# Kernel optimization log

Hardware: AMD Instinct MI355X
Metric: run time of the kernel (lower is better)

## Reference

```python
import jax, jax.numpy as jnp
import numpy as np

N, D, H = 3072, 1152, 16
HD = D // H  # 72


def setup_inputs() -> dict:
    key = jax.random.key(0)
    ks = jax.random.split(key, 12)
    w = lambda k, shp: jax.random.normal(k, shp, dtype=jnp.float32) * 0.02
    return {
        "hidden_states": jax.random.normal(ks[0], (N, D), dtype=jnp.float32),
        "rotary_pos_emb": jax.random.normal(ks[1], (N, HD // 2), dtype=jnp.float32),
        "cu_seqlens": jnp.arange(5, dtype=jnp.int32) * (N // 4),
        "wq": w(ks[2], (D, D)), "bq": jnp.zeros((D,), jnp.float32),
        "wk": w(ks[3], (D, D)), "bk": jnp.zeros((D,), jnp.float32),
        "wv": w(ks[4], (D, D)), "bv": jnp.zeros((D,), jnp.float32),
        "wo": w(ks[5], (D, D)), "bo": jnp.zeros((D,), jnp.float32),
    }


def _rotate_half(x):
    x1, x2 = jnp.split(x, 2, axis=-1)
    return jnp.concatenate((-x2, x1), axis=-1)


def _apply_rope(t, freqs):
    # t: [N, H, HD], freqs: [N, HD//2]
    cos = jnp.concatenate([jnp.cos(freqs), jnp.cos(freqs)], axis=-1)[:, None, :]  # [N,1,HD]
    sin = jnp.concatenate([jnp.sin(freqs), jnp.sin(freqs)], axis=-1)[:, None, :]
    return (t.astype(jnp.float32) * cos + _rotate_half(t.astype(jnp.float32)) * sin).astype(t.dtype)


def reference(hidden_states, rotary_pos_emb, cu_seqlens, wq, bq, wk, bk, wv, bv, wo, bo):
    n = hidden_states.shape[0]
    q = (hidden_states @ wq.T + bq).reshape(n, H, HD)
    k = (hidden_states @ wk.T + bk).reshape(n, H, HD)
    v = (hidden_states @ wv.T + bv).reshape(n, H, HD)
    q = _apply_rope(q, rotary_pos_emb)
    k = _apply_rope(k, rotary_pos_emb)
    # block-diagonal mask: same segment id (from cu_seqlens) -> attend
    seg = jnp.searchsorted(cu_seqlens, jnp.arange(n), side="right")
    same = seg[:, None] == seg[None, :]  # [N, N]
    neg = jnp.finfo(q.dtype).min
    scores = jnp.einsum("qhd,khd->hqk", q, k) / jnp.sqrt(jnp.float32(HD)).astype(q.dtype)
    scores = scores + jnp.where(same, jnp.zeros((), q.dtype), neg)[None, :, :]
    attn = jax.nn.softmax(scores.astype(jnp.float32), axis=-1).astype(q.dtype)
    out = jnp.einsum("hqk,khd->qhd", attn, v).reshape(n, D)
    return out @ wo.T + bo
```

## Files before the change

### kernel.cpp

```cpp
#include <hip/hip_runtime.h>
#include <hip/hip_bf16.h>


typedef __attribute__((ext_vector_type(8))) __bf16 bf16x8;
typedef __attribute__((ext_vector_type(4))) float f32x4;
typedef __attribute__((ext_vector_type(8))) unsigned short u16x8;
typedef __attribute__((ext_vector_type(4))) unsigned short u16x4;
typedef __attribute__((ext_vector_type(4))) unsigned int u32x4;

#define N_TOK 3072
#define DMODEL 1152
#define NH 16
#define HDIM 72
#define SEGLEN 768

__device__ __forceinline__ unsigned short bf16rn(float f) {
  union { float f; unsigned int u; } v; v.f = f;
  return (unsigned short)((v.u + 0x7fffu + ((v.u >> 16) & 1u)) >> 16);
}
__device__ __forceinline__ float bf2f(unsigned short u) {
  union { unsigned int i; float f; } v; v.i = ((unsigned int)u) << 16;
  return v.f;
}

#define GLOAD16(gsrc, ldst)                                                  \
  __builtin_amdgcn_global_load_lds(                                         \
      (const __attribute__((address_space(1))) unsigned int*)(gsrc),        \
      (__attribute__((address_space(3))) unsigned int*)(ldst), 16, 0, 0)

template <int N> __device__ __forceinline__ void waitcnt_vm() {
  if constexpr (N == 0) asm volatile("s_waitcnt vmcnt(0)" ::: "memory");
  else if constexpr (N == 3) asm volatile("s_waitcnt vmcnt(3)" ::: "memory");
  else if constexpr (N == 4) asm volatile("s_waitcnt vmcnt(4)" ::: "memory");
}

__global__ __launch_bounds__(256) void prep_kernel(
    const float* __restrict__ hs, const float* __restrict__ rope,
    const float* __restrict__ wq, const float* __restrict__ wk,
    const float* __restrict__ wv, const float* __restrict__ wo,
    const float* __restrict__ bq, const float* __restrict__ bk,
    const float* __restrict__ bv,
    unsigned short* __restrict__ Xbf, unsigned short* __restrict__ Wqkv,
    unsigned short* __restrict__ Wo, float* __restrict__ biasqkv,
    float* __restrict__ csT, float* __restrict__ snT) {
  const int idx = blockIdx.x * 256 + threadIdx.x;
  const int stride = gridDim.x * 256;
  const int NX4 = (N_TOK * DMODEL) / 4;
  const int NW4 = (DMODEL * DMODEL) / 4;
  for (int i = idx; i < NX4; i += stride) {
    f32x4 v = ((const f32x4*)hs)[i];
    u16x4 o;
    for (int j = 0; j < 4; ++j) o[j] = bf16rn(v[j]);
    ((u16x4*)Xbf)[i] = o;
  }
  for (int i = idx; i < NW4; i += stride) {
    f32x4 a = ((const f32x4*)wq)[i];
    f32x4 b = ((const f32x4*)wk)[i];
    f32x4 c = ((const f32x4*)wv)[i];
    f32x4 d = ((const f32x4*)wo)[i];
    u16x4 oa, ob, oc, od;
    for (int j = 0; j < 4; ++j) {
      oa[j] = bf16rn(a[j]); ob[j] = bf16rn(b[j]);
      oc[j] = bf16rn(c[j]); od[j] = bf16rn(d[j]);
    }
    ((u16x4*)Wqkv)[i] = oa;
    ((u16x4*)(Wqkv + DMODEL * DMODEL))[i] = ob;
    ((u16x4*)(Wqkv + 2 * DMODEL * DMODEL))[i] = oc;
    ((u16x4*)Wo)[i] = od;
  }
  for (int i = idx; i < N_TOK * 36; i += stride) {
    const int n = i / 36, d = i - n * 36;
    const float f = rope[i];
    csT[n * 40 + d] = __cosf(f);
    snT[n * 40 + d] = __sinf(f);
  }
  for (int i = idx; i < DMODEL; i += stride) {
    biasqkv[i] = bq[i];
    biasqkv[DMODEL + i] = bk[i];
    biasqkv[2 * DMODEL + i] = bv[i];
  }
}

template <int BM, int BN, int FM, int FN, bool OBF>
__global__ __launch_bounds__(256) void gemm_lds_kernel(
    const unsigned short* __restrict__ A, const unsigned short* __restrict__ B,
    const float* __restrict__ bias, void* __restrict__ Cout,
    int Nout, int K, int nbx) {
  __shared__ unsigned short As[3][BM * 32];
  __shared__ unsigned short Bs[3][BN * 32];
  const int t = threadIdx.x;
  const int lane = t & 63, wave = t >> 6;
  const int wr = wave >> 1, wc = wave & 1;
  const int g = lane >> 4, li = lane & 15;
  constexpr int LPS = BM / 64 + BN / 64;

  const int per = gridDim.x >> 3;
  const int gb = (blockIdx.x & 7) * per + (blockIdx.x >> 3);
  const int by = gb / nbx, bx = gb - by * nbx;
  const int bm = by * BM, bn = bx * BN;

  constexpr int LA = BM / 64;
  constexpr int LB = BN / 64;

  auto stage = [&](int buf, int kt) {
#pragma unroll
    for (int i = 0; i < LA; ++i) {
      const int s = i * 256 + t;
      const int row = s >> 2, cs = s & 3;
      const int gg = cs ^ ((row >> 1) & 3);
      GLOAD16(A + (long)(bm + row) * K + kt + gg * 8,
              &As[buf][(i * 256 + (t & ~63)) * 8]);
    }
#pragma unroll
    for (int i = 0; i < LB; ++i) {
      const int s = i * 256 + t;
      const int row = s >> 2, cs = s & 3;
      const int gg = cs ^ ((row >> 1) & 3);
      GLOAD16(B + (long)(bn + row) * K + kt + gg * 8,
              &Bs[buf][(i * 256 + (t & ~63)) * 8]);
    }
  };

  f32x4 acc[FM][FN];
#pragma unroll
  for (int i = 0; i < FM; ++i)
#pragma unroll
    for (int j = 0; j < FN; ++j) acc[i][j] = (f32x4)0.f;

  stage(0, 0);
  stage(1, 32);
  int cur = 0;
  const int nk = K / 32;
  for (int kt = 0; kt < nk; ++kt) {
    if (kt < nk - 1) waitcnt_vm<LPS>();
    else waitcnt_vm<0>();
    __builtin_amdgcn_s_barrier();
    if (kt + 2 < nk) {
      int nb = cur + 2; if (nb >= 3) nb -= 3;
      stage(nb, (kt + 2) * 32);
    }
    bf16x8 af[FM], bf[FN];
#pragma unroll
    for (int i = 0; i < FM; ++i) {
      const int r = wr * (BM / 2) + i * 16 + li;
      af[i] = *(const bf16x8*)&As[cur][r * 32 + ((g ^ ((r >> 1) & 3)) * 8)];
    }
#pragma unroll
    for (int j = 0; j < FN; ++j) {
      const int r = wc * (BN / 2) + j * 16 + li;
      bf[j] = *(const bf16x8*)&Bs[cur][r * 32 + ((g ^ ((r >> 1) & 3)) * 8)];
    }
    __builtin_amdgcn_s_setprio(1);
#pragma unroll
    for (int i = 0; i < FM; ++i)
#pragma unroll
      for (int j = 0; j < FN; ++j)
        acc[i][j] = __builtin_amdgcn_mfma_f32_16x16x32_bf16(af[i], bf[j],
                                                            acc[i][j], 0, 0, 0);
    __builtin_amdgcn_s_setprio(0);
    cur = (cur == 2) ? 0 : cur + 1;
  }

#pragma unroll
  for (int i = 0; i < FM; ++i) {
    const int row = bm + wr * (BM / 2) + i * 16 + g * 4;
#pragma unroll
    for (int j = 0; j < FN; ++j) {
      const int col = bn + wc * (BN / 2) + j * 16 + li;
      const float bb = bias[col];
#pragma unroll
      for (int r = 0; r < 4; ++r) {
        const float v = acc[i][j][r] + bb;
        if constexpr (OBF)
          ((unsigned short*)Cout)[(long)(row + r) * Nout + col] = bf16rn(v);
        else
          ((float*)Cout)[(long)(row + r) * Nout + col] = v;
      }
    }
  }
}

__global__ __launch_bounds__(256) void rope_pack_kernel(
    const unsigned short* __restrict__ qkv, const float* __restrict__ csT,
    const float* __restrict__ snT, unsigned short* __restrict__ Qp,
    unsigned short* __restrict__ Kp, unsigned short* __restrict__ Vt) {
  const int nb = blockIdx.x;
  const int h = blockIdx.y;
  const int n0 = nb * 64;
  const int t = threadIdx.x;
  const float qscale = 0.17002501f;
  __shared__ float vtile[72][65];

  for (int i = t; i < 64 * 9; i += 256) {
    const int n = i / 9, dq = (i % 9) * 4;
    const long base = (long)(n0 + n) * 3456 + h * HDIM;
    f32x4 cv = *(const f32x4*)&csT[(long)(n0 + n) * 40 + dq];
    f32x4 sv = *(const f32x4*)&snT[(long)(n0 + n) * 40 + dq];
    u16x4 q1 = *(const u16x4*)&qkv[base + dq];
    u16x4 q2 = *(const u16x4*)&qkv[base + dq + 36];
    u16x4 k1 = *(const u16x4*)&qkv[base + DMODEL + dq];
    u16x4 k2 = *(const u16x4*)&qkv[base + DMODEL + dq + 36];
    u16x4 oq1, oq2, ok1, ok2;
#pragma unroll
    for (int e = 0; e < 4; ++e) {
      const float c = cv[e], s = sv[e];
      float f1 = bf2f(q1[e]), f2 = bf2f(q2[e]);
      oq1[e] = bf16rn((f1 * c - f2 * s) * qscale);
      oq2[e] = bf16rn((f2 * c + f1 * s) * qscale);
      f1 = bf2f(k1[e]); f2 = bf2f(k2[e]);
      ok1[e] = bf16rn(f1 * c - f2 * s);
      ok2[e] = bf16rn(f2 * c + f1 * s);
    }
    const long ob = ((long)h * N_TOK + n0 + n) * 96;
    *(u16x4*)&Qp[ob + dq] = oq1;
    *(u16x4*)&Qp[ob + dq + 36] = oq2;
    *(u16x4*)&Kp[ob + dq] = ok1;
    *(u16x4*)&Kp[ob + dq + 36] = ok2;
  }
  for (int i = t; i < 64 * 6; i += 256) {
    const int n = i / 6, dp = HDIM + (i % 6) * 4;
    const long ob = ((long)h * N_TOK + n0 + n) * 96;
    *(u16x4*)&Qp[ob + dp] = (u16x4)0;
    *(u16x4*)&Kp[ob + dp] = (u16x4)0;
  }
  for (int i = t; i < 64 * 9; i += 256) {
    const int n = i / 9, dq = (i % 9) * 8;
    u16x8 v = *(const u16x8*)&qkv[(long)(n0 + n) * 3456 + 2 * DMODEL + h * HDIM + dq];
#pragma unroll
    for (int e = 0; e < 8; ++e) vtile[dq + e][n] = bf2f(v[e]);
  }
  __syncthreads();
  for (int i = t; i < 80 * 8; i += 256) {
    const int d = i / 8, nq = (i % 8) * 8;
    u16x8 o;
#pragma unroll
    for (int e = 0; e < 8; ++e)
      o[e] = (d < HDIM) ? bf16rn(vtile[d][nq + e])
                        : (d == HDIM ? (unsigned short)0x3F80
                                     : (unsigned short)0);
    *(u16x8*)&Vt[((long)h * 80 + d) * N_TOK + n0 + nq] = o;
  }
}

__global__ __launch_bounds__(256) void attn_kernel(
    const unsigned short* __restrict__ Qp, const unsigned short* __restrict__ Kp,
    const unsigned short* __restrict__ Vt, unsigned short* __restrict__ AO) {
  const int b = blockIdx.x;
  const int hs = b & 63, qt = b >> 6;
  const int h = hs >> 2, seg = hs & 3;
  const int t = threadIdx.x;
  const int lane = t & 63, w = t >> 6;
  const int g = lane >> 4, li = lane & 15;

  __shared__ unsigned short Ks[2][32 * 96];
  __shared__ unsigned short Vs[2][80 * 32];

  const int q0 = seg * SEGLEN + qt * 64;
  const unsigned short* kbase = Kp + ((long)h * N_TOK + seg * SEGLEN) * 96;
  const unsigned short* vbase = Vt + (long)h * 80 * N_TOK + seg * SEGLEN;

  auto stageK = [&](int buf, int koff) {
    {
      const int row = t / 12, c = t - row * 12;
      const int gg = c ^ ((row >> 1) & 3);
      GLOAD16(kbase + (long)(koff + row) * 96 + gg * 8,
              &Ks[buf][(t & ~63) * 8]);
    }
    if (t < 128) {
      const int s = 256 + t;
      const int row = s / 12, c = s - row * 12;
      const int gg = c ^ ((row >> 1) & 3);
      GLOAD16(kbase + (long)(koff + row) * 96 + gg * 8,
              &Ks[buf][(256 + (t & ~63)) * 8]);
    }
  };
  auto stageV = [&](int buf, int koff) {
    {
      const int row = t >> 2, ch = t & 3;
      const int gg = ch ^ ((row >> 1) & 3);
      GLOAD16(vbase + (long)row * N_TOK + koff + gg * 8,
              &Vs[buf][(t & ~63) * 8]);
    }
    if (t < 64) {
      const int s = 256 + t;
      const int row = s >> 2, ch = s & 3;
      const int gg = ch ^ ((row >> 1) & 3);
      GLOAD16(vbase + (long)row * N_TOK + koff + gg * 8,
              &Vs[buf][(256 + (t & ~63)) * 8]);
    }
  };

  bf16x8 aq[3];
  {
    const unsigned short* qsrc = Qp + ((long)h * N_TOK + q0 + w * 16 + li) * 96;
#pragma unroll
    for (int c = 0; c < 3; ++c)
      aq[c] = *(const bf16x8*)(qsrc + c * 32 + g * 8);
  }

  const int a0 = (li + 32 * (g & 1)) << 2;
  const int a1 = a0 + 64;
  const bool glow = (g < 2);

  f32x4 accO[5];
#pragma unroll
  for (int j = 0; j < 5; ++j) accO[j] = (f32x4)0.f;

  stageK(0, 0);
  stageV(0, 0);
  int cur = 0;
  for (int kv = 0; kv < 24; ++kv) {
    __syncthreads();
    if (kv + 1 < 24) {
      stageK(cur ^ 1, (kv + 1) * 32);
      stageV(cur ^ 1, (kv + 1) * 32);
    }

    f32x4 sc[2];
#pragma unroll
    for (int f = 0; f < 2; ++f) sc[f] = (f32x4)0.f;
    __builtin_amdgcn_s_setprio(1);
#pragma unroll
    for (int c = 0; c < 3; ++c)
#pragma unroll
      for (int f = 0; f < 2; ++f) {
        const int kr = f * 16 + li;
        bf16x8 bk = *(const bf16x8*)
            &Ks[cur][kr * 96 + (((c * 4 + g) ^ ((kr >> 1) & 3)) * 8)];
        sc[f] = __builtin_amdgcn_mfma_f32_16x16x32_bf16(bk, aq[c], sc[f], 0, 0, 0);
      }
    __builtin_amdgcn_s_setprio(0);

    float p00 = exp2f(sc[0][0]), p01 = exp2f(sc[0][1]);
    float p02 = exp2f(sc[0][2]), p03 = exp2f(sc[0][3]);
    float p10 = exp2f(sc[1][0]), p11 = exp2f(sc[1][1]);
    float p12 = exp2f(sc[1][2]), p13 = exp2f(sc[1][3]);
    unsigned int pk00, pk01, pk10, pk11;
    asm("v_cvt_pk_bf16_f32 %0, %1, %2" : "=v"(pk00) : "v"(p00), "v"(p01));
    asm("v_cvt_pk_bf16_f32 %0, %1, %2" : "=v"(pk01) : "v"(p02), "v"(p03));
    asm("v_cvt_pk_bf16_f32 %0, %1, %2" : "=v"(pk10) : "v"(p10), "v"(p11));
    asm("v_cvt_pk_bf16_f32 %0, %1, %2" : "=v"(pk11) : "v"(p12), "v"(p13));

    u32x4 apv;
    {
      int t0 = __builtin_amdgcn_ds_bpermute(a0, (int)pk00);
      int t1 = __builtin_amdgcn_ds_bpermute(a0, (int)pk10);
      apv[0] = (unsigned int)(glow ? t0 : t1);
      t0 = __builtin_amdgcn_ds_bpermute(a0, (int)pk01);
      t1 = __builtin_amdgcn_ds_bpermute(a0, (int)pk11);
      apv[1] = (unsigned int)(glow ? t0 : t1);
      t0 = __builtin_amdgcn_ds_bpermute(a1, (int)pk00);
      t1 = __builtin_amdgcn_ds_bpermute(a1, (int)pk10);
      apv[2] = (unsigned int)(glow ? t0 : t1);
      t0 = __builtin_amdgcn_ds_bpermute(a1, (int)pk01);
      t1 = __builtin_amdgcn_ds_bpermute(a1, (int)pk11);
      apv[3] = (unsigned int)(glow ? t0 : t1);
    }
    bf16x8 ap = *(bf16x8*)&apv;

    {
      __builtin_amdgcn_s_setprio(1);
#pragma unroll
      for (int j = 0; j < 5; ++j) {
        const int vr = j * 16 + li;
        bf16x8 bv = *(const bf16x8*)
            &Vs[cur][vr * 32 + ((g ^ ((vr >> 1) & 3)) * 8)];
        accO[j] = __builtin_amdgcn_mfma_f32_16x16x32_bf16(ap, bv, accO[j], 0, 0, 0);
      }
      __builtin_amdgcn_s_setprio(0);
    }
    cur ^= 1;
  }

  float rinv[4];
#pragma unroll
  for (int r = 0; r < 4; ++r)
    rinv[r] = 1.f / __shfl(accO[4][r], (lane & 48) + 8);

  const int hb = h * HDIM;
#pragma unroll
  for (int j = 0; j < 5; ++j) {
    const int d = j * 16 + li;
    if (d < HDIM) {
#pragma unroll
      for (int r = 0; r < 4; ++r) {
        const int n = q0 + w * 16 + g * 4 + r;
        AO[(long)n * DMODEL + hb + d] = bf16rn(accO[j][r] * rinv[r]);
      }
    }
  }
}

extern "C" void kernel_launch(void* const* d_in, const int* in_sizes, int n_in,
                              void* d_out, int out_size, void* d_ws,
                              size_t ws_size, hipStream_t stream) {
  const float* hs = (const float*)d_in[0];
  const float* rope = (const float*)d_in[1];
  const float* wq = (const float*)d_in[3];
  const float* bq = (const float*)d_in[4];
  const float* wk = (const float*)d_in[5];
  const float* bk = (const float*)d_in[6];
  const float* wv = (const float*)d_in[7];
  const float* bv = (const float*)d_in[8];
  const float* wo = (const float*)d_in[9];
  const float* bo = (const float*)d_in[10];
  float* out = (float*)d_out;
  char* ws = (char*)d_ws;

  unsigned short* Xbf = (unsigned short*)(ws + 0);
  unsigned short* Wqkv = (unsigned short*)(ws + 7077888);
  unsigned short* Wo = (unsigned short*)(ws + 15040512);
  float* biasqkv = (float*)(ws + 17694720);
  unsigned short* qkvb = (unsigned short*)(ws + 17708544);
  unsigned short* Qp = (unsigned short*)(ws + 38942208);
  unsigned short* Kp = (unsigned short*)(ws + 48379392);
  unsigned short* Vt = (unsigned short*)(ws + 57816576);
  unsigned short* AO = (unsigned short*)(ws + 65680896);
  float* csT = (float*)(ws + 72758784);
  float* snT = (float*)(ws + 73250304);

  prep_kernel<<<dim3(1024), dim3(256), 0, stream>>>(
      hs, rope, wq, wk, wv, wo, bq, bk, bv, Xbf, Wqkv, Wo, biasqkv, csT, snT);
  gemm_lds_kernel<128, 128, 4, 4, true><<<dim3(648), dim3(256), 0, stream>>>(
      Xbf, Wqkv, biasqkv, qkvb, 3 * DMODEL, DMODEL, 27);
  rope_pack_kernel<<<dim3(48, 16), dim3(256), 0, stream>>>(
      qkvb, csT, snT, Qp, Kp, Vt);
  attn_kernel<<<dim3(768), dim3(256), 0, stream>>>(Qp, Kp, Vt, AO);
  gemm_lds_kernel<64, 128, 2, 4, false><<<dim3(432), dim3(256), 0, stream>>>(
      AO, Wo, bo, out, DMODEL, DMODEL, 9);
}
```

Baseline: 107.4 us.

## Fuse RoPE and Q/K/V packing into QKV GEMM epilogue

Removes the separate rope_pack kernel and the intermediate qkv buffer. The Q and K weight rows are permuted so each rotary pair lands in adjacent columns, letting the GEMM epilogue apply RoPE with a lane shuffle and write directly to padded Qp/Kp and transposed Vt. Padding and the ones-row are written in the prep kernel instead. This trades an extra launch and a global round trip for scattered 2-byte stores from the epilogue, notably the uncoalesced transposed V writes.

```diff
diff --git a/kernel.cpp b/kernel.cpp
--- a/kernel.cpp
+++ b/kernel.cpp
@@ -21,6 +21,10 @@
 __device__ __forceinline__ float bf2f(unsigned short u) {
   union { unsigned int i; float f; } v; v.i = ((unsigned int)u) << 16;
   return v.f;
+}
+__device__ __forceinline__ int rope_perm(int rq) {
+  const int h = rq / HDIM, dd = rq - h * HDIM;
+  return h * HDIM + ((dd < 36) ? (2 * dd) : (2 * (dd - 36) + 1));
 }
 
 #define GLOAD16(gsrc, ldst)                                                  \
@@ -42,7 +46,9 @@
     const float* __restrict__ bv,
     unsigned short* __restrict__ Xbf, unsigned short* __restrict__ Wqkv,
     unsigned short* __restrict__ Wo, float* __restrict__ biasqkv,
-    float* __restrict__ csT, float* __restrict__ snT) {
+    float* __restrict__ csT, float* __restrict__ snT,
+    unsigned short* __restrict__ Qp, unsigned short* __restrict__ Kp,
+    unsigned short* __restrict__ Vt) {
   const int idx = blockIdx.x * 256 + threadIdx.x;
   const int stride = gridDim.x * 256;
   const int NX4 = (N_TOK * DMODEL) / 4;
@@ -54,6 +60,8 @@
     ((u16x4*)Xbf)[i] = o;
   }
   for (int i = idx; i < NW4; i += stride) {
+    const int rq = i / 288, c4 = i - rq * 288;
+    const int nr = rope_perm(rq);
     f32x4 a = ((const f32x4*)wq)[i];
     f32x4 b = ((const f32x4*)wk)[i];
     f32x4 c = ((const f32x4*)wv)[i];
@@ -63,8 +71,8 @@
       oa[j] = bf16rn(a[j]); ob[j] = bf16rn(b[j]);
       oc[j] = bf16rn(c[j]); od[j] = bf16rn(d[j]);
     }
-    ((u16x4*)Wqkv)[i] = oa;
-    ((u16x4*)(Wqkv + DMODEL * DMODEL))[i] = ob;
+    ((u16x4*)Wqkv)[nr * 288 + c4] = oa;
+    ((u16x4*)(Wqkv + DMODEL * DMODEL))[nr * 288 + c4] = ob;
     ((u16x4*)(Wqkv + 2 * DMODEL * DMODEL))[i] = oc;
     ((u16x4*)Wo)[i] = od;
   }
@@ -75,17 +83,34 @@
     snT[n * 40 + d] = __sinf(f);
   }
   for (int i = idx; i < DMODEL; i += stride) {
-    biasqkv[i] = bq[i];
-    biasqkv[DMODEL + i] = bk[i];
+    biasqkv[rope_perm(i)] = bq[i];
+    biasqkv[DMODEL + rope_perm(i)] = bk[i];
     biasqkv[2 * DMODEL + i] = bv[i];
   }
-}
-
-template <int BM, int BN, int FM, int FN, bool OBF>
+  for (int i = idx; i < NH * N_TOK * 6; i += stride) {
+    const int row = i / 6, q4 = i - row * 6;
+    *(u16x4*)&Qp[(long)row * 96 + 72 + q4 * 4] = (u16x4)0;
+    *(u16x4*)&Kp[(long)row * 96 + 72 + q4 * 4] = (u16x4)0;
+  }
+  for (int i = idx; i < NH * 8 * (N_TOK / 8); i += stride) {
+    const int hh = i / (8 * 384), rem = i - hh * 8 * 384;
+    const int dr = rem / 384, n8 = rem - dr * 384;
+    const unsigned short fill = (dr == 0) ? (unsigned short)0x3F80 : 0;
+    u16x8 o;
+#pragma unroll
+    for (int e = 0; e < 8; ++e) o[e] = fill;
+    *(u16x8*)&Vt[((long)(hh * 80 + 72 + dr)) * N_TOK + n8 * 8] = o;
+  }
+}
+
+template <int BM, int BN, int FM, int FN, int MODE>
 __global__ __launch_bounds__(256) void gemm_lds_kernel(
     const unsigned short* __restrict__ A, const unsigned short* __restrict__ B,
     const float* __restrict__ bias, void* __restrict__ Cout,
-    int Nout, int K, int nbx) {
+    int Nout, int K, int nbx,
+    unsigned short* __restrict__ Qp, unsigned short* __restrict__ Kp,
+    unsigned short* __restrict__ Vt, const float* __restrict__ csT,
+    const float* __restrict__ snT) {
   __shared__ unsigned short As[3][BM * 32];
   __shared__ unsigned short Bs[3][BN * 32];
   const int t = threadIdx.x;
@@ -161,84 +186,66 @@
     cur = (cur == 2) ? 0 : cur + 1;
   }
 
-#pragma unroll
-  for (int i = 0; i < FM; ++i) {
-    const int row = bm + wr * (BM / 2) + i * 16 + g * 4;
-#pragma unroll
-    for (int j = 0; j < FN; ++j) {
-      const int col = bn + wc * (BN / 2) + j * 16 + li;
-      const float bb = bias[col];
-#pragma unroll
-      for (int r = 0; r < 4; ++r) {
-        const float v = acc[i][j][r] + bb;
-        if constexpr (OBF)
-          ((unsigned short*)Cout)[(long)(row + r) * Nout + col] = bf16rn(v);
-        else
-          ((float*)Cout)[(long)(row + r) * Nout + col] = v;
-      }
-    }
-  }
-}
-
-__global__ __launch_bounds__(256) void rope_pack_kernel(
-    const unsigned short* __restrict__ qkv, const float* __restrict__ csT,
-    const float* __restrict__ snT, unsigned short* __restrict__ Qp,
-    unsigned short* __restrict__ Kp, unsigned short* __restrict__ Vt) {
-  const int nb = blockIdx.x;
-  const int h = blockIdx.y;
-  const int n0 = nb * 64;
-  const int t = threadIdx.x;
-  const float qscale = 0.17002501f;
-  __shared__ float vtile[72][65];
-
-  for (int i = t; i < 64 * 9; i += 256) {
-    const int n = i / 9, dq = (i % 9) * 4;
-    const long base = (long)(n0 + n) * 3456 + h * HDIM;
-    f32x4 cv = *(const f32x4*)&csT[(long)(n0 + n) * 40 + dq];
-    f32x4 sv = *(const f32x4*)&snT[(long)(n0 + n) * 40 + dq];
-    u16x4 q1 = *(const u16x4*)&qkv[base + dq];
-    u16x4 q2 = *(const u16x4*)&qkv[base + dq + 36];
-    u16x4 k1 = *(const u16x4*)&qkv[base + DMODEL + dq];
-    u16x4 k2 = *(const u16x4*)&qkv[base + DMODEL + dq + 36];
-    u16x4 oq1, oq2, ok1, ok2;
-#pragma unroll
-    for (int e = 0; e < 4; ++e) {
-      const float c = cv[e], s = sv[e];
-      float f1 = bf2f(q1[e]), f2 = bf2f(q2[e]);
-      oq1[e] = bf16rn((f1 * c - f2 * s) * qscale);
-      oq2[e] = bf16rn((f2 * c + f1 * s) * qscale);
-      f1 = bf2f(k1[e]); f2 = bf2f(k2[e]);
-      ok1[e] = bf16rn(f1 * c - f2 * s);
-      ok2[e] = bf16rn(f2 * c + f1 * s);
-    }
-    const long ob = ((long)h * N_TOK + n0 + n) * 96;
-    *(u16x4*)&Qp[ob + dq] = oq1;
-    *(u16x4*)&Qp[ob + dq + 36] = oq2;
-    *(u16x4*)&Kp[ob + dq] = ok1;
-    *(u16x4*)&Kp[ob + dq + 36] = ok2;
-  }
-  for (int i = t; i < 64 * 6; i += 256) {
-    const int n = i / 6, dp = HDIM + (i % 6) * 4;
-    const long ob = ((long)h * N_TOK + n0 + n) * 96;
-    *(u16x4*)&Qp[ob + dp] = (u16x4)0;
-    *(u16x4*)&Kp[ob + dp] = (u16x4)0;
-  }
-  for (int i = t; i < 64 * 9; i += 256) {
-    const int n = i / 9, dq = (i % 9) * 8;
-    u16x8 v = *(const u16x8*)&qkv[(long)(n0 + n) * 3456 + 2 * DMODEL + h * HDIM + dq];
-#pragma unroll
-    for (int e = 0; e < 8; ++e) vtile[dq + e][n] = bf2f(v[e]);
-  }
-  __syncthreads();
-  for (int i = t; i < 80 * 8; i += 256) {
-    const int d = i / 8, nq = (i % 8) * 8;
-    u16x8 o;
-#pragma unroll
-    for (int e = 0; e < 8; ++e)
-      o[e] = (d < HDIM) ? bf16rn(vtile[d][nq + e])
-                        : (d == HDIM ? (unsigned short)0x3F80
-                                     : (unsigned short)0);
-    *(u16x8*)&Vt[((long)h * 80 + d) * N_TOK + n0 + nq] = o;
+  if constexpr (MODE == 0) {
+#pragma unroll
+    for (int i = 0; i < FM; ++i) {
+      const int row = bm + wr * (BM / 2) + i * 16 + g * 4;
+#pragma unroll
+      for (int j = 0; j < FN; ++j) {
+        const int col = bn + wc * (BN / 2) + j * 16 + li;
+        const float bb = bias[col];
+#pragma unroll
+        for (int r = 0; r < 4; ++r)
+          ((float*)Cout)[(long)(row + r) * Nout + col] = acc[i][j][r] + bb;
+      }
+    }
+  } else {
+    const int part = bn / DMODEL;
+    const int pcol0 = bn - part * DMODEL;
+    if (part < 2) {
+      unsigned short* dst = (part == 0) ? Qp : Kp;
+      const float qs = (part == 0) ? 0.17002501f : 1.0f;
+#pragma unroll
+      for (int i = 0; i < FM; ++i) {
+        const int row0 = bm + wr * (BM / 2) + i * 16 + g * 4;
+#pragma unroll
+        for (int j = 0; j < FN; ++j) {
+          const int colp = pcol0 + wc * (BN / 2) + j * 16 + li;
+          const int h = colp / HDIM;
+          const int e = colp - h * HDIM;
+          const int jj = e >> 1, odd = e & 1;
+          const int d = jj + odd * 36;
+          const float bb = bias[bn + wc * (BN / 2) + j * 16 + li];
+#pragma unroll
+          for (int r = 0; r < 4; ++r) {
+            const int n = row0 + r;
+            const float val = acc[i][j][r] + bb;
+            const float par = __shfl_xor(val, 1);
+            const float c = csT[n * 40 + jj], s = snT[n * 40 + jj];
+            const float out = (odd ? (val * c + par * s)
+                                   : (val * c - par * s)) * qs;
+            dst[((long)(h * N_TOK + n)) * 96 + d] = bf16rn(out);
+          }
+        }
+      }
+    } else {
+#pragma unroll
+      for (int i = 0; i < FM; ++i) {
+        const int row0 = bm + wr * (BM / 2) + i * 16 + g * 4;
+#pragma unroll
+        for (int j = 0; j < FN; ++j) {
+          const int colp = pcol0 + wc * (BN / 2) + j * 16 + li;
+          const int h = colp / HDIM;
+          const int d = colp - h * HDIM;
+          const float bb = bias[bn + wc * (BN / 2) + j * 16 + li];
+#pragma unroll
+          for (int r = 0; r < 4; ++r) {
+            const int n = row0 + r;
+            Vt[((long)(h * 80 + d)) * N_TOK + n] = bf16rn(acc[i][j][r] + bb);
+          }
+        }
+      }
+    }
   }
 }
 
@@ -411,7 +418,6 @@
   unsigned short* Wqkv = (unsigned short*)(ws + 7077888);
   unsigned short* Wo = (unsigned short*)(ws + 15040512);
   float* biasqkv = (float*)(ws + 17694720);
-  unsigned short* qkvb = (unsigned short*)(ws + 17708544);
   unsigned short* Qp = (unsigned short*)(ws + 38942208);
   unsigned short* Kp = (unsigned short*)(ws + 48379392);
   unsigned short* Vt = (unsigned short*)(ws + 57816576);
@@ -420,12 +426,13 @@
   float* snT = (float*)(ws + 73250304);
 
   prep_kernel<<<dim3(1024), dim3(256), 0, stream>>>(
-      hs, rope, wq, wk, wv, wo, bq, bk, bv, Xbf, Wqkv, Wo, biasqkv, csT, snT);
-  gemm_lds_kernel<128, 128, 4, 4, true><<<dim3(648), dim3(256), 0, stream>>>(
-      Xbf, Wqkv, biasqkv, qkvb, 3 * DMODEL, DMODEL, 27);
-  rope_pack_kernel<<<dim3(48, 16), dim3(256), 0, stream>>>(
-      qkvb, csT, snT, Qp, Kp, Vt);
+      hs, rope, wq, wk, wv, wo, bq, bk, bv, Xbf, Wqkv, Wo, biasqkv,
+      csT, snT, Qp, Kp, Vt);
+  gemm_lds_kernel<128, 128, 4, 4, 1><<<dim3(648), dim3(256), 0, stream>>>(
+      Xbf, Wqkv, biasqkv, nullptr, 3 * DMODEL, DMODEL, 27,
+      Qp, Kp, Vt, csT, snT);
   attn_kernel<<<dim3(768), dim3(256), 0, stream>>>(Qp, Kp, Vt, AO);
-  gemm_lds_kernel<64, 128, 2, 4, false><<<dim3(432), dim3(256), 0, stream>>>(
-      AO, Wo, bo, out, DMODEL, DMODEL, 9);
-}
+  gemm_lds_kernel<64, 128, 2, 4, 0><<<dim3(432), dim3(256), 0, stream>>>(
+      AO, Wo, bo, out, DMODEL, DMODEL, 9,
+      nullptr, nullptr, nullptr, nullptr, nullptr);
+}
```

New measurement: 122.7 us. 1.14x slower.
